# Kernel optimization log

Hardware: AMD Instinct MI355X
Metric: run time of the kernel (lower is better)

## Reference

```python
import jax, jax.numpy as jnp
import numpy as np

EPS = 1e-12  # matches torch F.normalize eps


def _l2norm(t):
    n = jnp.linalg.norm(t, axis=-1, keepdims=True)
    return t / jnp.maximum(n, EPS)


def setup_inputs() -> dict:
    key = jax.random.key(0)
    ks = jax.random.split(key, 10)
    B, N, C = 2, 2048, 384
    nH, hd = 12, 32
    inp = {
        "x": jax.random.normal(ks[0], (B, N, C), jnp.float32),
        "q_w": jax.random.normal(ks[1], (C, C), jnp.float32) * 0.02,
        "q_b": jax.random.normal(ks[2], (C,), jnp.float32) * 0.02,
        "kv_w": jax.random.normal(ks[3], (2 * C, C), jnp.float32) * 0.02,
        "kv_b": jax.random.normal(ks[4], (2 * C,), jnp.float32) * 0.02,
        "query_embedding": jax.random.normal(ks[5], (nH, 1, hd), jnp.float32) * 0.02,
        # init of temperature in torch: log(exp(1/0.24) - 1)
        "temperature": jnp.full((nH, 1, 1), float(np.log(np.exp(1.0 / 0.24) - 1.0)), jnp.float32),
        "pos_bias": jax.random.normal(ks[7], (nH, N), jnp.float32) * 0.0004,
        "proj_w": jax.random.normal(ks[8], (C, C), jnp.float32) * 0.02,
        "proj_b": jax.random.normal(ks[9], (C,), jnp.float32) * 0.02,
        "D": 8, "H": 16, "W": 16,
    }
    return inp


def reference(x, q_w, q_b, kv_w, kv_b, query_embedding, temperature, pos_bias, proj_w, proj_b, D, H, W):
    B, N, C = x.shape
    nH, hd = query_embedding.shape[0], query_embedding.shape[2]
    assert N == D * H * W
    # q projection -> [B, nH, N, hd], cosine-normalized
    q = (x @ q_w.T + q_b).reshape(B, N, nH, hd).transpose(0, 2, 1, 3)
    q = _l2norm(q)
    # additive query embedding, softplus temperature, seq-length (log N) scale
    scale = jax.nn.softplus(temperature) * jnp.float32(np.log(N))  # [nH,1,1]
    q = (q + query_embedding[None]) * scale[None]
    # kv projection
    kv = x @ kv_w.T + kv_b  # [B, N, 2C]
    k, v = kv[..., :C], kv[..., C:]
    k = _l2norm(k.reshape(B, N, nH, hd).transpose(0, 2, 1, 3))
    v = v.reshape(B, N, nH, hd).transpose(0, 2, 1, 3)
    # scores with per-head learned positional bias over keys
    attn = jnp.einsum("bhqd,bhkd->bhqk", q, k) + pos_bias[None, :, None, :]
    attn = jax.nn.softmax(attn, axis=-1)
    out = jnp.einsum("bhqk,bhkd->bhqd", attn, v)
    out = out.transpose(0, 2, 1, 3).reshape(B, N, C)
    return out @ proj_w.T + proj_b
```

## Files before the change

kernel.cpp:

```cpp
#include <hip/hip_runtime.h>

#define LOG2E 1.4426950408889634f

typedef __bf16 bf16x8 __attribute__((ext_vector_type(8)));
typedef short s16x4 __attribute__((ext_vector_type(4)));
typedef float f32x4 __attribute__((ext_vector_type(4)));

#define BB 2
#define NN 2048
#define CC 384
#define NH 12
#define HD 32
#define MROWS (BB * NN)

__device__ __forceinline__ unsigned short f2bf(float f) {
  __bf16 h = (__bf16)f;
  return __builtin_bit_cast(unsigned short, h);
}

__device__ __forceinline__ bf16x8 ldg_bf8(const unsigned short* p) {
  uint4 v = *reinterpret_cast<const uint4*>(p);
  return __builtin_bit_cast(bf16x8, v);
}

typedef __attribute__((address_space(1))) const void gas_void;
typedef __attribute__((address_space(3))) void las_void;
__device__ __forceinline__ void gload_lds16(const void* g, void* l) {
  __builtin_amdgcn_global_load_lds((gas_void*)(unsigned long long)g,
                                   (las_void*)(unsigned long long)l, 16, 0, 0);
}

__device__ __forceinline__ f32x4 mfma32(bf16x8 a, bf16x8 b, f32x4 c) {
  return __builtin_amdgcn_mfma_f32_16x16x32_bf16(a, b, c, 0, 0, 0);
}

__device__ __forceinline__ f32x4 mfma16(s16x4 a, s16x4 b, f32x4 c) {
#if defined(__HIP_DEVICE_COMPILE__)
#if __has_builtin(__builtin_amdgcn_mfma_f32_16x16x16bf16_1k)
  return __builtin_amdgcn_mfma_f32_16x16x16bf16_1k(a, b, c, 0, 0, 0);
#else
  asm volatile("v_mfma_f32_16x16x16_bf16 %0, %1, %2, %0"
               : "+v"(c) : "v"(a), "v"(b));
  return c;
#endif
#else
  return c;
#endif
}

__global__ __launch_bounds__(256) void prep_kernel(
    const float* __restrict__ x, const float* __restrict__ q_w,
    const float* __restrict__ kv_w, const float* __restrict__ proj_w,
    unsigned short* __restrict__ xb, unsigned short* __restrict__ qwb,
    unsigned short* __restrict__ kvwb, unsigned short* __restrict__ pwb) {
  int i = blockIdx.x * 256 + threadIdx.x;
  if (i < 1572864) { xb[i] = f2bf(x[i]); return; }
  i -= 1572864;
  if (i < 147456) { qwb[i] = f2bf(q_w[i]); return; }
  i -= 147456;
  if (i < 294912) { kvwb[i] = f2bf(kv_w[i]); return; }
  i -= 294912;
  pwb[i] = f2bf(proj_w[i]);
}

__global__ __launch_bounds__(256, 4) void gemm_qkv_norm_kernel(
    const unsigned short* __restrict__ xb, const unsigned short* __restrict__ qwb,
    const unsigned short* __restrict__ kvwb, const float* __restrict__ q_b,
    const float* __restrict__ kv_b, const float* __restrict__ qe,
    const float* __restrict__ temperature, unsigned short* __restrict__ Qs,
    unsigned short* __restrict__ Kn, unsigned short* __restrict__ VT) {
  __shared__ alignas(16) char smem[2][20480];
  int wave = threadIdx.x >> 6, lane = threadIdx.x & 63;
  int c = lane & 15, quad = lane >> 4;
  int h = blockIdx.y;
  int m0b = blockIdx.x * 64;
  int cid = wave * 64 + lane;

  auto stage = [&](int buf, int kk) {
    char* base = smem[buf];
#pragma unroll
    for (int j = 0; j < 2; ++j) {
      int chunk = j * 256 + cid;
      int row = chunk >> 3, e = chunk & 7;
      gload_lds16(xb + (long)(m0b + row) * CC + kk + e * 8,
                  base + j * 4096 + wave * 1024);
    }
#pragma unroll
    for (int j = 0; j < 3; ++j) {
      int chunk = j * 256 + cid;
      int row = chunk >> 3, e = chunk & 7;
      const unsigned short* src;
      if (row < 32)      src = qwb + (long)(h * 32 + row) * CC;
      else if (row < 64) src = kvwb + (long)(h * 32 + (row - 32)) * CC;
      else               src = kvwb + (long)(CC + h * 32 + (row - 64)) * CC;
      gload_lds16(src + kk + e * 8, base + 8192 + j * 4096 + wave * 1024);
    }
  };

  f32x4 acc[6] = {};
  auto compute = [&](int buf) {
    const char* base = smem[buf];
#pragma unroll
    for (int kh = 0; kh < 2; ++kh) {
      bf16x8 a = *(const bf16x8*)(base + (wave * 16 + c) * 128 + kh * 64 + quad * 16);
#pragma unroll
      for (int t = 0; t < 6; ++t) {
        bf16x8 b = *(const bf16x8*)(base + 8192 + (t * 16 + c) * 128 + kh * 64 + quad * 16);
        acc[t] = mfma32(a, b, acc[t]);
      }
    }
  };

  stage(0, 0);
#pragma unroll 1
  for (int s = 0; s < 6; ++s) {
    __syncthreads();
    if (s < 5) stage((s + 1) & 1, (s + 1) * 64);
    compute(s & 1);
  }

  int m0 = m0b + wave * 16;
  float qb0 = q_b[h * 32 + c], qb1 = q_b[h * 32 + 16 + c];
  float kb0 = kv_b[h * 32 + c], kb1 = kv_b[h * 32 + 16 + c];
  float vb0 = kv_b[CC + h * 32 + c], vb1 = kv_b[CC + h * 32 + 16 + c];
  float qe0 = qe[h * HD + c], qe1 = qe[h * HD + 16 + c];
  float sc = log1pf(expf(temperature[h])) * 11.0f;
  int b = m0 >> 11;
  int nb = (m0 & 2047) + quad * 4;
  int pair = b * NH + h;
  unsigned short* qsb = Qs + ((long)pair * NN + nb) * HD;
  unsigned short* knb = Kn + ((long)pair * NN + nb) * HD;
  ushort4 vp0, vp1;
#pragma unroll
  for (int r = 0; r < 4; ++r) {
    float q0 = acc[0][r] + qb0, q1 = acc[1][r] + qb1;
    float k0 = acc[2][r] + kb0, k1 = acc[3][r] + kb1;
    float v0 = acc[4][r] + vb0, v1 = acc[5][r] + vb1;
    float qs = q0 * q0 + q1 * q1, ks = k0 * k0 + k1 * k1;
#pragma unroll
    for (int off = 8; off; off >>= 1) {
      qs += __shfl_xor(qs, off);
      ks += __shfl_xor(ks, off);
    }
    float qi = 1.0f / fmaxf(sqrtf(qs), 1e-12f);
    float ki = 1.0f / fmaxf(sqrtf(ks), 1e-12f);
    qsb[r * HD + c] = f2bf((q0 * qi + qe0) * sc);
    qsb[r * HD + 16 + c] = f2bf((q1 * qi + qe1) * sc);
    knb[r * HD + c] = f2bf(k0 * ki);
    knb[r * HD + 16 + c] = f2bf(k1 * ki);
    ((unsigned short*)&vp0)[r] = f2bf(v0);
    ((unsigned short*)&vp1)[r] = f2bf(v1);
  }
  *reinterpret_cast<ushort4*>(VT + ((long)pair * HD + c) * NN + nb) = vp0;
  *reinterpret_cast<ushort4*>(VT + ((long)pair * HD + 16 + c) * NN + nb) = vp1;
}

__global__ __launch_bounds__(256, 4) void attn_kernel(
    const unsigned short* __restrict__ Qs, const unsigned short* __restrict__ Kn,
    const unsigned short* __restrict__ VT, const float* __restrict__ pos_bias,
    unsigned short* __restrict__ ao) {
  __shared__ alignas(16) char smem[2][16384];
  int wave = threadIdx.x >> 6, lane = threadIdx.x & 63;
  int c = lane & 15, quad = lane >> 4;
  int pair = blockIdx.y, h = pair % NH, b = pair / NH;
  const unsigned short* Qp = Qs + (long)pair * NN * HD;
  const unsigned short* Kp = Kn + (long)pair * NN * HD;
  const unsigned short* Vp = VT + (long)pair * HD * NN;
  const float* bp = pos_bias + h * NN;
  int q0 = blockIdx.x * 64 + wave * 16;
  bf16x8 qf = ldg_bf8(Qp + (long)(q0 + c) * HD + quad * 8);
  f32x4 o0 = {}, o1 = {};
  float rs = 0.f;
  int cid = wave * 64 + lane;

  auto stage = [&](int buf, int k0) {
    char* base = smem[buf];
    const char* Kg = (const char*)Kp + (long)k0 * (HD * 2);
    const char* Vg = (const char*)Vp + (long)k0 * 2;
#pragma unroll
    for (int j = 0; j < 2; ++j) {
      int chunk = j * 256 + cid;
      gload_lds16(Kg + chunk * 16, base + j * 4096 + wave * 1024);
      int d = chunk >> 4, e = chunk & 15;
      int es = e ^ (d & 15);
      gload_lds16(Vg + (long)d * (NN * 2) + es * 16,
                  base + 8192 + j * 4096 + wave * 1024);
    }
  };

  auto compute = [&](int buf, int k0) {
    const char* kb = smem[buf];
    const char* vb = smem[buf] + 8192;
#pragma unroll
    for (int t8 = 0; t8 < 8; ++t8) {
      bf16x8 kf = *(const bf16x8*)(kb + (t8 * 16 + c) * 64 + quad * 16);
      f32x4 z = {};
      f32x4 s = mfma32(kf, qf, z);
      f32x4 bb = *(const f32x4*)(bp + k0 + t8 * 16 + quad * 4);
      float p0 = exp2f(fmaf(bb[0], LOG2E, s[0]));
      float p1 = exp2f(fmaf(bb[1], LOG2E, s[1]));
      float p2 = exp2f(fmaf(bb[2], LOG2E, s[2]));
      float p3 = exp2f(fmaf(bb[3], LOG2E, s[3]));
      rs += (p0 + p1) + (p2 + p3);
      s16x4 pf = {(short)f2bf(p0), (short)f2bf(p1),
                  (short)f2bf(p2), (short)f2bf(p3)};
      int vsw = (((t8 * 2 + (quad >> 1)) ^ c) * 16) + (quad & 1) * 8;
      s16x4 vlo = *(const s16x4*)(vb + c * 256 + vsw);
      s16x4 vhi = *(const s16x4*)(vb + (c + 16) * 256 + vsw);
      o0 = mfma16(vlo, pf, o0);
      o1 = mfma16(vhi, pf, o1);
    }
  };

  stage(0, 0);
#pragma unroll 1
  for (int it = 0; it < 16; ++it) {
    __syncthreads();
    if (it < 15) stage((it + 1) & 1, (it + 1) * 128);
    compute(it & 1, it * 128);
  }

  rs += __shfl_xor(rs, 16);
  rs += __shfl_xor(rs, 32);
  float inv = 1.0f / rs;
  unsigned short* op = ao + (long)(b * NN + q0 + c) * CC + h * HD + quad * 4;
  ushort4 s0, s1;
#pragma unroll
  for (int r = 0; r < 4; ++r) {
    ((unsigned short*)&s0)[r] = f2bf(o0[r] * inv);
    ((unsigned short*)&s1)[r] = f2bf(o1[r] * inv);
  }
  *reinterpret_cast<ushort4*>(op) = s0;
  *reinterpret_cast<ushort4*>(op + 16) = s1;
}

__global__ __launch_bounds__(256, 4) void proj_kernel(
    const unsigned short* __restrict__ ab, const unsigned short* __restrict__ pwb,
    const float* __restrict__ proj_b, float* __restrict__ out) {
  __shared__ alignas(16) char smem[2][16384];
  int wave = threadIdx.x >> 6, lane = threadIdx.x & 63;
  int c = lane & 15, quad = lane >> 4;
  int m0b = blockIdx.x * 64;
  int n0 = blockIdx.y * 64;
  int cid = wave * 64 + lane;

  auto stage = [&](int buf, int kk) {
    char* base = smem[buf];
#pragma unroll
    for (int j = 0; j < 2; ++j) {
      int chunk = j * 256 + cid;
      int row = chunk >> 3, e = chunk & 7;
      gload_lds16(ab + (long)(m0b + row) * CC + kk + e * 8,
                  base + j * 4096 + wave * 1024);
      gload_lds16(pwb + (long)(n0 + row) * CC + kk + e * 8,
                  base + 8192 + j * 4096 + wave * 1024);
    }
  };

  f32x4 acc[4] = {};
  auto compute = [&](int buf) {
    const char* base = smem[buf];
#pragma unroll
    for (int kh = 0; kh < 2; ++kh) {
      bf16x8 a = *(const bf16x8*)(base + (wave * 16 + c) * 128 + kh * 64 + quad * 16);
#pragma unroll
      for (int t = 0; t < 4; ++t) {
        bf16x8 b = *(const bf16x8*)(base + 8192 + (t * 16 + c) * 128 + kh * 64 + quad * 16);
        acc[t] = mfma32(a, b, acc[t]);
      }
    }
  };

  stage(0, 0);
#pragma unroll 1
  for (int s = 0; s < 6; ++s) {
    __syncthreads();
    if (s < 5) stage((s + 1) & 1, (s + 1) * 64);
    compute(s & 1);
  }

  int m0 = m0b + wave * 16;
#pragma unroll
  for (int t = 0; t < 4; ++t) {
    int o = n0 + t * 16 + c;
    float bv = proj_b[o];
#pragma unroll
    for (int r = 0; r < 4; ++r) {
      out[(long)(m0 + quad * 4 + r) * CC + o] = acc[t][r] + bv;
    }
  }
}

extern "C" void kernel_launch(void* const* d_in, const int* in_sizes, int n_in,
                              void* d_out, int out_size, void* d_ws, size_t ws_size,
                              hipStream_t stream) {
  const float* x = (const float*)d_in[0];
  const float* q_w = (const float*)d_in[1];
  const float* q_b = (const float*)d_in[2];
  const float* kv_w = (const float*)d_in[3];
  const float* kv_b = (const float*)d_in[4];
  const float* qe = (const float*)d_in[5];
  const float* temp = (const float*)d_in[6];
  const float* pos_bias = (const float*)d_in[7];
  const float* proj_w = (const float*)d_in[8];
  const float* proj_b = (const float*)d_in[9];
  float* out = (float*)d_out;

  char* ws = (char*)d_ws;
  unsigned short* xb = (unsigned short*)(ws + 0);
  unsigned short* qwb = (unsigned short*)(ws + 3145728);
  unsigned short* kvwb = (unsigned short*)(ws + 3440640);
  unsigned short* pwb = (unsigned short*)(ws + 4030464);
  unsigned short* Qs = (unsigned short*)(ws + 4325376);
  unsigned short* Kn = (unsigned short*)(ws + 7471104);
  unsigned short* VT = (unsigned short*)(ws + 10616832);
  unsigned short* ao = (unsigned short*)(ws + 13762560);

  prep_kernel<<<8448, 256, 0, stream>>>(x, q_w, kv_w, proj_w, xb, qwb, kvwb, pwb);
  gemm_qkv_norm_kernel<<<dim3(64, NH), 256, 0, stream>>>(xb, qwb, kvwb, q_b, kv_b,
                                                         qe, temp, Qs, Kn, VT);
  attn_kernel<<<dim3(32, 24), 256, 0, stream>>>(Qs, Kn, VT, pos_bias, ao);
  proj_kernel<<<dim3(64, 6), 256, 0, stream>>>(ao, pwb, proj_b, out);
}
```

Measured before the change: 147.3 us.

## Restage K/V tiles in fragment-order LDS layout, use native exp2 and packed bf16 convert

```diff
diff --git a/kernel.cpp b/kernel.cpp
--- a/kernel.cpp
+++ b/kernel.cpp
@@ -21,6 +21,27 @@
 __device__ __forceinline__ bf16x8 ldg_bf8(const unsigned short* p) {
   uint4 v = *reinterpret_cast<const uint4*>(p);
   return __builtin_bit_cast(bf16x8, v);
+}
+
+__device__ __forceinline__ float fexp2(float x) {
+#if __has_builtin(__builtin_amdgcn_exp2f)
+  return __builtin_amdgcn_exp2f(x);
+#else
+  return exp2f(x);
+#endif
+}
+
+__device__ __forceinline__ s16x4 pack_bf4(float a, float b, float c, float d) {
+#if __has_builtin(__builtin_amdgcn_cvt_pk_bf16_f32)
+  auto lo = __builtin_amdgcn_cvt_pk_bf16_f32(a, b);
+  auto hi = __builtin_amdgcn_cvt_pk_bf16_f32(c, d);
+  uint2 u = {__builtin_bit_cast(unsigned int, lo),
+             __builtin_bit_cast(unsigned int, hi)};
+  return __builtin_bit_cast(s16x4, u);
+#else
+  s16x4 r = {(short)f2bf(a), (short)f2bf(b), (short)f2bf(c), (short)f2bf(d)};
+  return r;
+#endif
 }
 
 typedef __attribute__((address_space(1))) const void gas_void;
@@ -164,49 +185,49 @@
   int c = lane & 15, quad = lane >> 4;
   int pair = blockIdx.y, h = pair % NH, b = pair / NH;
   const unsigned short* Qp = Qs + (long)pair * NN * HD;
-  const unsigned short* Kp = Kn + (long)pair * NN * HD;
-  const unsigned short* Vp = VT + (long)pair * HD * NN;
+  const char* Kg0 = (const char*)(Kn + (long)pair * NN * HD);
+  const char* Vg0 = (const char*)(VT + (long)pair * HD * NN);
   const float* bp = pos_bias + h * NN;
   int q0 = blockIdx.x * 64 + wave * 16;
   bf16x8 qf = ldg_bf8(Qp + (long)(q0 + c) * HD + quad * 8);
   f32x4 o0 = {}, o1 = {};
   float rs = 0.f;
-  int cid = wave * 64 + lane;
+
+  const int koff = (c * 4 + quad) * 16;
+  const int voff = (lane & 31) * (NN * 2) + (lane >> 5) * 16;
+  const int vro = (quad >> 1) * 512 + (quad & 1) * 8 + c * 16;
 
   auto stage = [&](int buf, int k0) {
     char* base = smem[buf];
-    const char* Kg = (const char*)Kp + (long)k0 * (HD * 2);
-    const char* Vg = (const char*)Vp + (long)k0 * 2;
+    const char* Kg = Kg0 + (long)k0 * (HD * 2);
+    const char* Vg = Vg0 + (long)k0 * 2;
 #pragma unroll
     for (int j = 0; j < 2; ++j) {
-      int chunk = j * 256 + cid;
-      gload_lds16(Kg + chunk * 16, base + j * 4096 + wave * 1024);
-      int d = chunk >> 4, e = chunk & 15;
-      int es = e ^ (d & 15);
-      gload_lds16(Vg + (long)d * (NN * 2) + es * 16,
+      gload_lds16(Kg + (j * 4 + wave) * 1024 + koff,
+                  base + j * 4096 + wave * 1024);
+      gload_lds16(Vg + voff + j * 128 + wave * 32,
                   base + 8192 + j * 4096 + wave * 1024);
     }
   };
 
   auto compute = [&](int buf, int k0) {
-    const char* kb = smem[buf];
-    const char* vb = smem[buf] + 8192;
+    const char* kb = smem[buf] + lane * 16;
+    const char* vb = smem[buf] + 8192 + vro;
+    const float* bq = bp + k0 + quad * 4;
 #pragma unroll
     for (int t8 = 0; t8 < 8; ++t8) {
-      bf16x8 kf = *(const bf16x8*)(kb + (t8 * 16 + c) * 64 + quad * 16);
+      bf16x8 kf = *(const bf16x8*)(kb + t8 * 1024);
       f32x4 z = {};
       f32x4 s = mfma32(kf, qf, z);
-      f32x4 bb = *(const f32x4*)(bp + k0 + t8 * 16 + quad * 4);
-      float p0 = exp2f(fmaf(bb[0], LOG2E, s[0]));
-      float p1 = exp2f(fmaf(bb[1], LOG2E, s[1]));
-      float p2 = exp2f(fmaf(bb[2], LOG2E, s[2]));
-      float p3 = exp2f(fmaf(bb[3], LOG2E, s[3]));
+      f32x4 bbv = *(const f32x4*)(bq + t8 * 16);
+      float p0 = fexp2(fmaf(bbv[0], LOG2E, s[0]));
+      float p1 = fexp2(fmaf(bbv[1], LOG2E, s[1]));
+      float p2 = fexp2(fmaf(bbv[2], LOG2E, s[2]));
+      float p3 = fexp2(fmaf(bbv[3], LOG2E, s[3]));
       rs += (p0 + p1) + (p2 + p3);
-      s16x4 pf = {(short)f2bf(p0), (short)f2bf(p1),
-                  (short)f2bf(p2), (short)f2bf(p3)};
-      int vsw = (((t8 * 2 + (quad >> 1)) ^ c) * 16) + (quad & 1) * 8;
-      s16x4 vlo = *(const s16x4*)(vb + c * 256 + vsw);
-      s16x4 vhi = *(const s16x4*)(vb + (c + 16) * 256 + vsw);
+      s16x4 pf = pack_bf4(p0, p1, p2, p3);
+      s16x4 vlo = *(const s16x4*)(vb + t8 * 1024);
+      s16x4 vhi = *(const s16x4*)(vb + t8 * 1024 + 256);
       o0 = mfma16(vlo, pf, o0);
       o1 = mfma16(vhi, pf, o1);
     }
```

Result: slower. 158.7 us (+7.7%).
